# Kernel optimization log

Measured on AMD Instinct MI355X. Metric: run time of the kernel, lower is better.

Reference implementation:

```python
import jax, jax.numpy as jnp
import numpy as np

LN_EPS = 1e-5

def _layer_norm(x, g, b):
    mu = jnp.mean(x, axis=-1, keepdims=True)
    var = jnp.mean(jnp.square(x - mu), axis=-1, keepdims=True)
    return (x - mu) * jax.lax.rsqrt(var + LN_EPS) * g + b

def _conv(x, src, tgt, N, alphas, ws, W3, W_self, bias, deg_power):
    # alphas, ws: tuples of 3 per-edge [E] arrays (sp, ctx, lat)
    # W3: [3, in, out]; deg_power: [3]
    out = x @ W_self + bias  # self loop + bias, [N, out]
    for c in range(3):
        eff = alphas[c] * ws[c]                                   # [E]
        deg = jnp.ones((N,), x.dtype).at[tgt].add(eff)            # [N]
        dinv = jnp.power(jnp.clip(deg, 1e-6), deg_power[c])       # [N]
        norm = eff * dinv[tgt] * dinv[src]                        # [E]
        h = x @ W3[c]                                             # [N, out] (linear => transform before gather)
        msg = norm[:, None] * h[src]                              # [E, out]
        out = out + jax.ops.segment_sum(msg, tgt, num_segments=N)
    return out

def setup_inputs() -> dict:
    N, E, D, L = 50000, 1000000, 128, 2
    key = jax.random.key(0)
    ks = jax.random.split(key, 16)
    scale = 1.0 / np.sqrt(D)
    inp = {
        "x": jax.random.normal(ks[0], (N, D), jnp.float32),
        "edge_index": jax.random.randint(ks[1], (2, E), 0, N, jnp.int32),
        "alpha_sp": jax.random.uniform(ks[2], (E,), jnp.float32),
        "alpha_ctx": jax.random.uniform(ks[3], (E,), jnp.float32),
        "alpha_lat": jax.random.uniform(ks[4], (E,), jnp.float32),
        "w_sp": jax.random.uniform(ks[5], (E,), jnp.float32),
        "w_ctx": jax.random.uniform(ks[6], (E,), jnp.float32),
        "w_lat": jax.random.uniform(ks[7], (E,), jnp.float32),
        # stacked per-layer params: [L, 3, in, out] for the three channel weights
        "W3": jax.random.normal(ks[8], (L, 3, D, D), jnp.float32) * scale,
        "W_self": jax.random.normal(ks[9], (L, D, D), jnp.float32) * scale,
        "bias": jnp.zeros((L, D), jnp.float32),
        "deg_power": jnp.full((L, 3), -0.5, jnp.float32),
        "ln_g": jnp.ones((D,), jnp.float32),
        "ln_b": jnp.zeros((D,), jnp.float32),
        "num_nodes": N,
    }
    return inp

def reference(x, edge_index, alpha_sp, alpha_ctx, alpha_lat, w_sp, w_ctx, w_lat,
              W3, W_self, bias, deg_power, ln_g, ln_b, num_nodes):
    N = num_nodes
    src, tgt = edge_index[0], edge_index[1]
    alphas = (alpha_sp, alpha_ctx, alpha_lat)
    ws = (w_sp, w_ctx, w_lat)
    L = W3.shape[0]
    h = x
    for i in range(L):
        h = _conv(h, src, tgt, N, alphas, ws, W3[i], W_self[i], bias[i], deg_power[i])
        if i < L - 1:
            h = _layer_norm(h, ln_g, ln_b)
            h = jax.nn.relu(h)
            # dropout: eval mode (identity)
    return h
```

## Files before the change

kernel.cpp:

```cpp
#include <hip/hip_runtime.h>
#include <hip/hip_bf16.h>

typedef short bf16x8 __attribute__((ext_vector_type(8)));
typedef float f32x4 __attribute__((ext_vector_type(4)));

#define BSH 7
#define BK  (1 << BSH)

static inline int cdiv(int a, int b){ return (a + b - 1) / b; }

__device__ __forceinline__ unsigned pack_bf16_hi(float v){
    return ((unsigned)__bfloat16_as_ushort(__float2bfloat16(v))) << 16;
}
__device__ __forceinline__ float bf16hi_to_f32(unsigned bits_hi16){
    return __uint_as_float(bits_hi16);
}

__global__ __launch_bounds__(256) void k_bcnt0(const int* __restrict__ tgt,
                                               int* __restrict__ gcnt, int E, int NB){
    __shared__ int lh[1024];
    int tid = threadIdx.x;
    for (int b = tid; b < 1024; b += 256) lh[b] = 0;
    __syncthreads();
    int c0 = blockIdx.x * 4096;
    #pragma unroll
    for (int u = 0; u < 16; ++u){
        int e = c0 + u * 256 + tid;
        if (e < E) atomicAdd(&lh[tgt[e] >> BSH], 1);
    }
    __syncthreads();
    for (int b = tid; b < NB; b += 256){
        int c = lh[b];
        if (c) atomicAdd(&gcnt[b], c);
    }
}

__global__ __launch_bounds__(256) void k_bscan(const int* __restrict__ gcnt,
                                               int* __restrict__ bbase,
                                               int* __restrict__ gcur,
                                               int* __restrict__ rs,
                                               int N, int E){
    __shared__ int sc[256];
    int tid = threadIdx.x;
    int b0 = tid * 4;
    int v0 = gcnt[b0], v1 = gcnt[b0 + 1], v2 = gcnt[b0 + 2], v3 = gcnt[b0 + 3];
    int t3 = v0 + v1 + v2 + v3;
    sc[tid] = t3;
    __syncthreads();
    for (int off = 1; off < 256; off <<= 1){
        int x = (tid >= off) ? sc[tid - off] : 0;
        __syncthreads();
        sc[tid] += x;
        __syncthreads();
    }
    int ex = sc[tid] - t3;
    bbase[b0]     = ex;
    bbase[b0 + 1] = ex + v0;
    bbase[b0 + 2] = ex + v0 + v1;
    bbase[b0 + 3] = ex + v0 + v1 + v2;
    gcur[b0] = bbase[b0]; gcur[b0 + 1] = bbase[b0 + 1];
    gcur[b0 + 2] = bbase[b0 + 2]; gcur[b0 + 3] = bbase[b0 + 3];
    if (tid == 255) bbase[1024] = sc[255];
    if (tid == 0)   rs[N] = E;
}

__global__ __launch_bounds__(256) void k_bin(
        const int* __restrict__ src, const int* __restrict__ tgt,
        const float* __restrict__ asp, const float* __restrict__ actx,
        const float* __restrict__ alat, const float* __restrict__ wsp,
        const float* __restrict__ wctx, const float* __restrict__ wlat,
        int* __restrict__ gcur, uint4* __restrict__ binned, int E, int NB){
    __shared__ int lh[1024], lc[1024], gb[1024];
    int tid = threadIdx.x;
    int c0 = blockIdx.x * 4096;
    for (int b = tid; b < 1024; b += 256){ lh[b] = 0; lc[b] = 0; }
    __syncthreads();
    #pragma unroll
    for (int u = 0; u < 16; ++u){
        int e = c0 + u * 256 + tid;
        if (e < E) atomicAdd(&lh[tgt[e] >> BSH], 1);
    }
    __syncthreads();
    for (int b = tid; b < NB; b += 256){
        int c = lh[b];
        gb[b] = c ? atomicAdd(&gcur[b], c) : 0;
    }
    __syncthreads();
    #pragma unroll
    for (int u = 0; u < 16; ++u){
        int e = c0 + u * 256 + tid;
        if (e < E){
            int t = tgt[e];
            int b = t >> BSH;
            int p = gb[b] + atomicAdd(&lc[b], 1);
            uint4 o;
            o.x = (unsigned)src[e] | pack_bf16_hi(asp[e] * wsp[e]);
            o.y = (pack_bf16_hi(actx[e] * wctx[e]) >> 16) | pack_bf16_hi(alat[e] * wlat[e]);
            o.z = (unsigned)t;
            o.w = 0u;
            binned[p] = o;
        }
    }
}

__global__ __launch_bounds__(256) void k_bucket(
        const uint4* __restrict__ binned, const int* __restrict__ bbase,
        const float* __restrict__ dp,
        uint2* __restrict__ effo, int* __restrict__ rs,
        float* __restrict__ dinv_all,
        int N, int L){
    __shared__ int th[128], sc2[128], cur[128];
    __shared__ float sm[384];
    int tid = threadIdx.x;
    int b = blockIdx.x;
    int t0 = b << BSH;
    int ebeg = bbase[b], eend = bbase[b + 1];
    if (tid < 128) th[tid] = 0;
    for (int j = tid; j < 384; j += 256) sm[j] = 0.f;
    __syncthreads();
    for (int i = ebeg + tid; i < eend; i += 256)
        atomicAdd(&th[(int)binned[i].z - t0], 1);
    __syncthreads();
    int v = (tid < 128) ? th[tid] : 0;
    if (tid < 128) sc2[tid] = v;
    __syncthreads();
    for (int off = 1; off < 128; off <<= 1){
        int x = (tid >= off && tid < 128) ? sc2[tid - off] : 0;
        __syncthreads();
        if (tid < 128) sc2[tid] += x;
        __syncthreads();
    }
    if (tid < 128){
        int exv = sc2[tid] - v;
        cur[tid] = exv;
        int t = t0 + tid;
        if (t < N) rs[t] = ebeg + exv;
    }
    __syncthreads();
    for (int i = ebeg + tid; i < eend; i += 256){
        uint4 r = binned[i];
        int loc = (int)r.z - t0;
        int p = atomicAdd(&cur[loc], 1);
        uint2 o = {r.x, r.y};
        effo[ebeg + p] = o;
        atomicAdd(&sm[loc * 3 + 0], bf16hi_to_f32(r.x & 0xFFFF0000u));
        atomicAdd(&sm[loc * 3 + 1], bf16hi_to_f32(r.y << 16));
        atomicAdd(&sm[loc * 3 + 2], bf16hi_to_f32(r.y & 0xFFFF0000u));
    }
    __syncthreads();
    if (tid < 128){
        int t = t0 + tid;
        if (t < N){
            float d0 = fmaxf(1.f + sm[tid * 3 + 0], 1e-6f);
            float d1 = fmaxf(1.f + sm[tid * 3 + 1], 1e-6f);
            float d2 = fmaxf(1.f + sm[tid * 3 + 2], 1e-6f);
            for (int l = 0; l < L; ++l){
                size_t base = ((size_t)l * N + t) * 3;
                dinv_all[base + 0] = powf(d0, dp[l * 3 + 0]);
                dinv_all[base + 1] = powf(d1, dp[l * 3 + 1]);
                dinv_all[base + 2] = powf(d2, dp[l * 3 + 2]);
            }
        }
    }
}

__global__ void k_prep(const uint2* __restrict__ effo,
                       const float* __restrict__ dinv_all,
                       uint2* __restrict__ nv,
                       const float* __restrict__ x, __hip_bfloat16* __restrict__ xg,
                       const float* __restrict__ Wself, const float* __restrict__ W3,
                       __hip_bfloat16* __restrict__ BT,
                       int N, int E, int L){
    int gid = blockIdx.x * 256 + threadIdx.x;
    int LE = L * E;
    int nx4 = (N * 128) >> 2;
    int nw = L * 65536;
    if (gid < LE){
        int l = gid / E;
        int e = gid - l * E;
        const float* dinv = dinv_all + (size_t)l * N * 3;
        uint2 v = effo[e];
        unsigned s = v.x & 0xFFFFu;
        float e0 = bf16hi_to_f32(v.x & 0xFFFF0000u);
        float e1 = bf16hi_to_f32(v.y << 16);
        float e2 = bf16hi_to_f32(v.y & 0xFFFF0000u);
        uint2 o;
        o.x = s | pack_bf16_hi(e0 * dinv[3 * s + 0]);
        o.y = (pack_bf16_hi(e1 * dinv[3 * s + 1]) >> 16)
            | pack_bf16_hi(e2 * dinv[3 * s + 2]);
        nv[gid] = o;
    } else if (gid < LE + nx4){
        int i = gid - LE;
        float4 v = ((const float4*)x)[i];
        float2 lo = {v.x, v.y}, hi = {v.z, v.w};
        ((__hip_bfloat162*)xg)[2 * i]     = __float22bfloat162_rn(lo);
        ((__hip_bfloat162*)xg)[2 * i + 1] = __float22bfloat162_rn(hi);
    } else if (gid < LE + nx4 + nw){
        int q = gid - LE - nx4;
        int l = q >> 16, r = q & 65535;
        int j = r >> 9, k = r & 511;
        float v;
        if (k < 128) v = Wself[l * 16384 + k * 128 + j];
        else {
            int c = (k >> 7) - 1, kk = k & 127;
            v = W3[l * 49152 + (c * 128 + kk) * 128 + j];
        }
        BT[q] = __float2bfloat16(v);
    }
}

__global__ __launch_bounds__(256) void k_msg(
        const __hip_bfloat16* __restrict__ xg,
        __hip_bfloat16* __restrict__ Yg,
        const uint2* __restrict__ nv,
        const int* __restrict__ rs,
        const float* __restrict__ dinv,
        int N){
    int w = threadIdx.x >> 6, lane = threadIdx.x & 63;
    int t = blockIdx.x * 4 + w;
    if (t >= N) return;
    float ax0 = 0.f, ay0 = 0.f, ax1 = 0.f, ay1 = 0.f, ax2 = 0.f, ay2 = 0.f;
    int beg = rs[t], end = rs[t + 1];
    int i = beg;
    for (; i + 8 <= end; i += 8){
        uint2 m[8];
        #pragma unroll
        for (int u = 0; u < 8; ++u) m[u] = nv[i + u];
        float2 f[8];
        #pragma unroll
        for (int u = 0; u < 8; ++u){
            const __hip_bfloat162* p =
                (const __hip_bfloat162*)(xg + (size_t)(m[u].x & 0xFFFFu) * 128);
            f[u] = __bfloat1622float2(p[lane]);
        }
        #pragma unroll
        for (int u = 0; u < 8; ++u){
            float n0 = bf16hi_to_f32(m[u].x & 0xFFFF0000u);
            float n1 = bf16hi_to_f32(m[u].y << 16);
            float n2 = bf16hi_to_f32(m[u].y & 0xFFFF0000u);
            ax0 += n0 * f[u].x; ay0 += n0 * f[u].y;
            ax1 += n1 * f[u].x; ay1 += n1 * f[u].y;
            ax2 += n2 * f[u].x; ay2 += n2 * f[u].y;
        }
    }
    for (; i < end; ++i){
        uint2 m = nv[i];
        const __hip_bfloat162* p =
            (const __hip_bfloat162*)(xg + (size_t)(m.x & 0xFFFFu) * 128);
        float2 fv = __bfloat1622float2(p[lane]);
        float n0 = bf16hi_to_f32(m.x & 0xFFFF0000u);
        float n1 = bf16hi_to_f32(m.y << 16);
        float n2 = bf16hi_to_f32(m.y & 0xFFFF0000u);
        ax0 += n0 * fv.x; ay0 += n0 * fv.y;
        ax1 += n1 * fv.x; ay1 += n1 * fv.y;
        ax2 += n2 * fv.x; ay2 += n2 * fv.y;
    }
    float dt0 = dinv[3 * t], dt1 = dinv[3 * t + 1], dt2 = dinv[3 * t + 2];
    __hip_bfloat162* yo = (__hip_bfloat162*)(Yg + (size_t)t * 384) + lane;
    float2 r0 = {dt0 * ax0, dt0 * ay0};
    float2 r1 = {dt1 * ax1, dt1 * ay1};
    float2 r2 = {dt2 * ax2, dt2 * ay2};
    yo[0]   = __float22bfloat162_rn(r0);
    yo[64]  = __float22bfloat162_rn(r1);
    yo[128] = __float22bfloat162_rn(r2);
}

__global__ __launch_bounds__(256) void k_gemm(
        const __hip_bfloat16* __restrict__ Yg,
        const __hip_bfloat16* __restrict__ BT,
        const float* __restrict__ bias,
        float* __restrict__ outbuf,
        int M, int doLN,
        const float* __restrict__ g, const float* __restrict__ b,
        __hip_bfloat16* __restrict__ xg){
    __shared__ __hip_bfloat16 As[64 * 128];
    __shared__ __hip_bfloat16 Bs[128 * 128];
    const int tid = threadIdx.x;
    const int row0 = blockIdx.x * 64;
    const int w = tid >> 6, lane = tid & 63;
    const int wm = (w & 1) * 32, wn = (w >> 1) * 64;
    const int lm = lane & 15, lq = lane >> 4;

    f32x4 acc[2][4];
    #pragma unroll
    for (int mt = 0; mt < 2; ++mt)
        #pragma unroll
        for (int nt = 0; nt < 4; ++nt)
            acc[mt][nt] = {0.f, 0.f, 0.f, 0.f};

    for (int kt = 0; kt < 4; ++kt){
        #pragma unroll
        for (int it = 0; it < 4; ++it){
            int v = it * 256 + tid;
            int r = v >> 4, c = v & 15;
            int soff = r * 128 + ((c ^ (r & 15)) << 3);
            int4 av = {0, 0, 0, 0};
            if (row0 + r < M){
                if (kt == 0)
                    av = *(const int4*)(xg + (size_t)(row0 + r) * 128 + (c << 3));
                else
                    av = *(const int4*)(Yg + (size_t)(row0 + r) * 384
                                        + (kt - 1) * 128 + (c << 3));
            }
            *(int4*)(&As[soff]) = av;
        }
        #pragma unroll
        for (int it = 0; it < 8; ++it){
            int v = it * 256 + tid;
            int r = v >> 4, c = v & 15;
            int soff = r * 128 + ((c ^ (r & 15)) << 3);
            int4 bv = *(const int4*)(BT + (size_t)r * 512 + kt * 128 + (c << 3));
            *(int4*)(&Bs[soff]) = bv;
        }
        __syncthreads();

        #pragma unroll
        for (int kk = 0; kk < 4; ++kk){
            int kc = kk * 4 + lq;
            bf16x8 a[2], b2[4];
            #pragma unroll
            for (int mt = 0; mt < 2; ++mt){
                int r = wm + mt * 16 + lm;
                a[mt] = *(const bf16x8*)(&As[r * 128 + ((kc ^ (r & 15)) << 3)]);
            }
            #pragma unroll
            for (int nt = 0; nt < 4; ++nt){
                int r = wn + nt * 16 + lm;
                b2[nt] = *(const bf16x8*)(&Bs[r * 128 + ((kc ^ (r & 15)) << 3)]);
            }
            #pragma unroll
            for (int mt = 0; mt < 2; ++mt)
                #pragma unroll
                for (int nt = 0; nt < 4; ++nt)
                    acc[mt][nt] = __builtin_amdgcn_mfma_f32_16x16x32_bf16(
                        a[mt], b2[nt], acc[mt][nt], 0, 0, 0);
        }
        __syncthreads();
    }

    if (!doLN){
        #pragma unroll
        for (int mt = 0; mt < 2; ++mt){
            #pragma unroll
            for (int nt = 0; nt < 4; ++nt){
                int col = wn + nt * 16 + lm;
                #pragma unroll
                for (int r = 0; r < 4; ++r){
                    int row = row0 + wm + mt * 16 + lq * 4 + r;
                    if (row < M)
                        outbuf[(size_t)row * 128 + col] = acc[mt][nt][r] + bias[col];
                }
            }
        }
    } else {
        float* S1 = (float*)As;
        float* S2 = S1 + 2048;
        float* MS = (float*)Bs;
        const int half = wn >> 6;
        const int slot = half * 16 + lm;
        float bv[4];
        #pragma unroll
        for (int nt = 0; nt < 4; ++nt) bv[nt] = bias[wn + nt * 16 + lm];
        #pragma unroll
        for (int mt = 0; mt < 2; ++mt){
            #pragma unroll
            for (int r = 0; r < 4; ++r){
                int rl = wm + mt * 16 + lq * 4 + r;
                float ps = 0.f, pq = 0.f;
                #pragma unroll
                for (int nt = 0; nt < 4; ++nt){
                    float v = acc[mt][nt][r] + bv[nt];
                    ps += v; pq += v * v;
                }
                S1[rl * 32 + slot] = ps;
                S2[rl * 32 + slot] = pq;
            }
        }
        __syncthreads();
        if (tid < 64){
            float s = 0.f, sq = 0.f;
            #pragma unroll
            for (int j = 0; j < 32; ++j){
                s  += S1[tid * 32 + j];
                sq += S2[tid * 32 + j];
            }
            float mu = s * (1.0f / 128.0f);
            float var = sq * (1.0f / 128.0f) - mu * mu;
            MS[tid] = mu;
            MS[64 + tid] = rsqrtf(var + 1e-5f);
        }
        __syncthreads();
        float gv[4], bbv[4];
        #pragma unroll
        for (int nt = 0; nt < 4; ++nt){
            int col = wn + nt * 16 + lm;
            gv[nt] = g[col]; bbv[nt] = b[col];
        }
        #pragma unroll
        for (int mt = 0; mt < 2; ++mt){
            #pragma unroll
            for (int r = 0; r < 4; ++r){
                int rl = wm + mt * 16 + lq * 4 + r;
                int row = row0 + rl;
                if (row < M){
                    float mu = MS[rl], sc = MS[64 + rl];
                    #pragma unroll
                    for (int nt = 0; nt < 4; ++nt){
                        int col = wn + nt * 16 + lm;
                        float v = acc[mt][nt][r] + bv[nt];
                        float y = fmaxf((v - mu) * sc * gv[nt] + bbv[nt], 0.0f);
                        xg[(size_t)row * 128 + col] = __float2bfloat16(y);
                    }
                }
            }
        }
    }
}

extern "C" void kernel_launch(void* const* d_in, const int* in_sizes, int n_in,
                              void* d_out, int out_size, void* d_ws, size_t ws_size,
                              hipStream_t stream) {
    const float* x     = (const float*)d_in[0];
    const int*   ei    = (const int*)d_in[1];
    const float* asp   = (const float*)d_in[2];
    const float* actx  = (const float*)d_in[3];
    const float* alat  = (const float*)d_in[4];
    const float* wsp   = (const float*)d_in[5];
    const float* wctx  = (const float*)d_in[6];
    const float* wlat  = (const float*)d_in[7];
    const float* W3    = (const float*)d_in[8];
    const float* Wself = (const float*)d_in[9];
    const float* bias  = (const float*)d_in[10];
    const float* dpow  = (const float*)d_in[11];
    const float* lng   = (const float*)d_in[12];
    const float* lnb   = (const float*)d_in[13];

    const int N = in_sizes[0] / 128;
    const int E = in_sizes[1] / 2;
    const int L = in_sizes[8] / (3 * 128 * 128);
    const int NB = cdiv(N, BK);
    const int* src = ei;
    const int* tgt = ei + E;

    char* p = (char*)d_ws;
    auto alloc = [&](size_t bytes) -> void* {
        void* r = (void*)p;
        p += (bytes + 255) & ~(size_t)255;
        return r;
    };
    int*   rs       = (int*)  alloc((size_t)(N + 1) * 4);
    int*   gcnt     = (int*)  alloc(1024 * 4);
    int*   bbase    = (int*)  alloc(1025 * 4);
    int*   gcur     = (int*)  alloc(1024 * 4);
    uint2* effo     = (uint2*)alloc((size_t)E * 8);
    size_t nv_bytes = (size_t)L * E * 8, bn_bytes = (size_t)E * 16;
    uint2* nv       = (uint2*)alloc(nv_bytes > bn_bytes ? nv_bytes : bn_bytes);
    float* dinv_all = (float*)alloc((size_t)L * N * 3 * 4);
    __hip_bfloat16* xg = (__hip_bfloat16*)alloc((size_t)N * 128 * 2);
    __hip_bfloat16* Yg = (__hip_bfloat16*)alloc((size_t)N * 384 * 2);
    __hip_bfloat16* BT = (__hip_bfloat16*)alloc((size_t)L * 128 * 512 * 2);
    uint4* binned = (uint4*)nv;

    hipMemsetAsync(gcnt, 0, 1024 * 4, stream);
    k_bcnt0 <<<cdiv(E, 4096), 256, 0, stream>>>(tgt, gcnt, E, NB);
    k_bscan <<<1, 256, 0, stream>>>(gcnt, bbase, gcur, rs, N, E);
    k_bin   <<<cdiv(E, 4096), 256, 0, stream>>>(src, tgt, asp, actx, alat, wsp, wctx, wlat,
                                                gcur, binned, E, NB);
    k_bucket<<<NB, 256, 0, stream>>>(binned, bbase, dpow, effo, rs, dinv_all, N, L);
    {
        int total = L * E + ((N * 128) >> 2) + L * 65536;
        k_prep<<<cdiv(total, 256), 256, 0, stream>>>(effo, dinv_all, nv, x, xg,
                                                     Wself, W3, BT, N, E, L);
    }

    for (int l = 0; l < L; ++l){
        int doLN = (l < L - 1) ? 1 : 0;
        const float* dinv_l = dinv_all + (size_t)l * N * 3;
        k_msg <<<cdiv(N, 4), 256, 0, stream>>>(xg, Yg, nv + (size_t)l * E, rs, dinv_l, N);
        k_gemm<<<cdiv(N, 64), 256, 0, stream>>>(Yg, BT + (size_t)l * 65536,
                                                bias + l * 128, (float*)d_out, N,
                                                doLN, lng, lnb, xg);
    }
}
```

Measured before the change: 351.3 us.

## Replace two-level bucketed CSR build with direct per-node histogram, scan, scatter

Replaces the two-pass bucket binning (block-local histograms over 128-node buckets, then per-bucket sort with shared-memory degree sums) with a plain global atomic histogram over targets, a three-kernel prefix scan, a global-atomic scatter into CSR order, and a separate per-node degree kernel. This removes the intermediate 16-byte binned buffer and one full pass over it. In exchange it relies on global atomics spread across 50k counters, scatters with poor locality, and the degree kernel walks variable-length rows per thread. Edge order within a row is now nondeterministic, so the bf16 degree sums may vary slightly between runs.

```diff
diff --git a/kernel.cpp b/kernel.cpp
--- a/kernel.cpp
+++ b/kernel.cpp
@@ -4,9 +4,6 @@
 typedef short bf16x8 __attribute__((ext_vector_type(8)));
 typedef float f32x4 __attribute__((ext_vector_type(4)));
 
-#define BSH 7
-#define BK  (1 << BSH)
-
 static inline int cdiv(int a, int b){ return (a + b - 1) / b; }
 
 __device__ __forceinline__ unsigned pack_bf16_hi(float v){
@@ -16,34 +13,23 @@
     return __uint_as_float(bits_hi16);
 }
 
-__global__ __launch_bounds__(256) void k_bcnt0(const int* __restrict__ tgt,
-                                               int* __restrict__ gcnt, int E, int NB){
-    __shared__ int lh[1024];
-    int tid = threadIdx.x;
-    for (int b = tid; b < 1024; b += 256) lh[b] = 0;
-    __syncthreads();
-    int c0 = blockIdx.x * 4096;
-    #pragma unroll
-    for (int u = 0; u < 16; ++u){
-        int e = c0 + u * 256 + tid;
-        if (e < E) atomicAdd(&lh[tgt[e] >> BSH], 1);
-    }
-    __syncthreads();
-    for (int b = tid; b < NB; b += 256){
-        int c = lh[b];
-        if (c) atomicAdd(&gcnt[b], c);
-    }
-}
-
-__global__ __launch_bounds__(256) void k_bscan(const int* __restrict__ gcnt,
-                                               int* __restrict__ bbase,
-                                               int* __restrict__ gcur,
+__global__ __launch_bounds__(256) void k_hist(const int* __restrict__ tgt,
+                                              int* __restrict__ cnt, int E){
+    int stride = gridDim.x * 256;
+    for (int e = blockIdx.x * 256 + threadIdx.x; e < E; e += stride)
+        atomicAdd(&cnt[tgt[e]], 1);
+}
+
+__global__ __launch_bounds__(256) void k_scanA(const int* __restrict__ cnt,
                                                int* __restrict__ rs,
-                                               int N, int E){
+                                               int* __restrict__ part, int N){
     __shared__ int sc[256];
     int tid = threadIdx.x;
-    int b0 = tid * 4;
-    int v0 = gcnt[b0], v1 = gcnt[b0 + 1], v2 = gcnt[b0 + 2], v3 = gcnt[b0 + 3];
+    int base = blockIdx.x * 1024 + tid * 4;
+    int v0 = (base + 0 < N) ? cnt[base + 0] : 0;
+    int v1 = (base + 1 < N) ? cnt[base + 1] : 0;
+    int v2 = (base + 2 < N) ? cnt[base + 2] : 0;
+    int v3 = (base + 3 < N) ? cnt[base + 3] : 0;
     int t3 = v0 + v1 + v2 + v3;
     sc[tid] = t3;
     __syncthreads();
@@ -54,113 +40,74 @@
         __syncthreads();
     }
     int ex = sc[tid] - t3;
-    bbase[b0]     = ex;
-    bbase[b0 + 1] = ex + v0;
-    bbase[b0 + 2] = ex + v0 + v1;
-    bbase[b0 + 3] = ex + v0 + v1 + v2;
-    gcur[b0] = bbase[b0]; gcur[b0 + 1] = bbase[b0 + 1];
-    gcur[b0 + 2] = bbase[b0 + 2]; gcur[b0 + 3] = bbase[b0 + 3];
-    if (tid == 255) bbase[1024] = sc[255];
-    if (tid == 0)   rs[N] = E;
-}
-
-__global__ __launch_bounds__(256) void k_bin(
+    if (base + 0 < N) rs[base + 0] = ex;
+    if (base + 1 < N) rs[base + 1] = ex + v0;
+    if (base + 2 < N) rs[base + 2] = ex + v0 + v1;
+    if (base + 3 < N) rs[base + 3] = ex + v0 + v1 + v2;
+    if (tid == 255) part[blockIdx.x] = sc[255];
+}
+
+__global__ void k_scanB(int* __restrict__ part, int nb){
+    if (blockIdx.x == 0 && threadIdx.x == 0){
+        int acc = 0;
+        for (int i = 0; i < nb; ++i){ int t = part[i]; part[i] = acc; acc += t; }
+    }
+}
+
+__global__ __launch_bounds__(256) void k_scanC(int* __restrict__ rs,
+                                               int* __restrict__ cur,
+                                               const int* __restrict__ part,
+                                               int N, int E){
+    int i = blockIdx.x * 1024 + threadIdx.x * 4;
+    int b = part[blockIdx.x];
+    #pragma unroll
+    for (int u = 0; u < 4; ++u){
+        int j = i + u;
+        if (j < N){ int v = rs[j] + b; rs[j] = v; cur[j] = v; }
+    }
+    if (blockIdx.x == 0 && threadIdx.x == 0) rs[N] = E;
+}
+
+__global__ __launch_bounds__(256) void k_scatter(
         const int* __restrict__ src, const int* __restrict__ tgt,
         const float* __restrict__ asp, const float* __restrict__ actx,
         const float* __restrict__ alat, const float* __restrict__ wsp,
         const float* __restrict__ wctx, const float* __restrict__ wlat,
-        int* __restrict__ gcur, uint4* __restrict__ binned, int E, int NB){
-    __shared__ int lh[1024], lc[1024], gb[1024];
-    int tid = threadIdx.x;
-    int c0 = blockIdx.x * 4096;
-    for (int b = tid; b < 1024; b += 256){ lh[b] = 0; lc[b] = 0; }
-    __syncthreads();
-    #pragma unroll
-    for (int u = 0; u < 16; ++u){
-        int e = c0 + u * 256 + tid;
-        if (e < E) atomicAdd(&lh[tgt[e] >> BSH], 1);
-    }
-    __syncthreads();
-    for (int b = tid; b < NB; b += 256){
-        int c = lh[b];
-        gb[b] = c ? atomicAdd(&gcur[b], c) : 0;
-    }
-    __syncthreads();
-    #pragma unroll
-    for (int u = 0; u < 16; ++u){
-        int e = c0 + u * 256 + tid;
-        if (e < E){
-            int t = tgt[e];
-            int b = t >> BSH;
-            int p = gb[b] + atomicAdd(&lc[b], 1);
-            uint4 o;
-            o.x = (unsigned)src[e] | pack_bf16_hi(asp[e] * wsp[e]);
-            o.y = (pack_bf16_hi(actx[e] * wctx[e]) >> 16) | pack_bf16_hi(alat[e] * wlat[e]);
-            o.z = (unsigned)t;
-            o.w = 0u;
-            binned[p] = o;
-        }
-    }
-}
-
-__global__ __launch_bounds__(256) void k_bucket(
-        const uint4* __restrict__ binned, const int* __restrict__ bbase,
+        int* __restrict__ cur, uint2* __restrict__ effo, int E){
+    int stride = gridDim.x * 256;
+    for (int e = blockIdx.x * 256 + threadIdx.x; e < E; e += stride){
+        int t = tgt[e];
+        int p = atomicAdd(&cur[t], 1);
+        uint2 o;
+        o.x = (unsigned)src[e] | pack_bf16_hi(asp[e] * wsp[e]);
+        o.y = (pack_bf16_hi(actx[e] * wctx[e]) >> 16) | pack_bf16_hi(alat[e] * wlat[e]);
+        effo[p] = o;
+    }
+}
+
+__global__ __launch_bounds__(256) void k_deg(
+        const uint2* __restrict__ effo, const int* __restrict__ rs,
         const float* __restrict__ dp,
-        uint2* __restrict__ effo, int* __restrict__ rs,
         float* __restrict__ dinv_all,
         int N, int L){
-    __shared__ int th[128], sc2[128], cur[128];
-    __shared__ float sm[384];
-    int tid = threadIdx.x;
-    int b = blockIdx.x;
-    int t0 = b << BSH;
-    int ebeg = bbase[b], eend = bbase[b + 1];
-    if (tid < 128) th[tid] = 0;
-    for (int j = tid; j < 384; j += 256) sm[j] = 0.f;
-    __syncthreads();
-    for (int i = ebeg + tid; i < eend; i += 256)
-        atomicAdd(&th[(int)binned[i].z - t0], 1);
-    __syncthreads();
-    int v = (tid < 128) ? th[tid] : 0;
-    if (tid < 128) sc2[tid] = v;
-    __syncthreads();
-    for (int off = 1; off < 128; off <<= 1){
-        int x = (tid >= off && tid < 128) ? sc2[tid - off] : 0;
-        __syncthreads();
-        if (tid < 128) sc2[tid] += x;
-        __syncthreads();
-    }
-    if (tid < 128){
-        int exv = sc2[tid] - v;
-        cur[tid] = exv;
-        int t = t0 + tid;
-        if (t < N) rs[t] = ebeg + exv;
-    }
-    __syncthreads();
-    for (int i = ebeg + tid; i < eend; i += 256){
-        uint4 r = binned[i];
-        int loc = (int)r.z - t0;
-        int p = atomicAdd(&cur[loc], 1);
-        uint2 o = {r.x, r.y};
-        effo[ebeg + p] = o;
-        atomicAdd(&sm[loc * 3 + 0], bf16hi_to_f32(r.x & 0xFFFF0000u));
-        atomicAdd(&sm[loc * 3 + 1], bf16hi_to_f32(r.y << 16));
-        atomicAdd(&sm[loc * 3 + 2], bf16hi_to_f32(r.y & 0xFFFF0000u));
-    }
-    __syncthreads();
-    if (tid < 128){
-        int t = t0 + tid;
-        if (t < N){
-            float d0 = fmaxf(1.f + sm[tid * 3 + 0], 1e-6f);
-            float d1 = fmaxf(1.f + sm[tid * 3 + 1], 1e-6f);
-            float d2 = fmaxf(1.f + sm[tid * 3 + 2], 1e-6f);
-            for (int l = 0; l < L; ++l){
-                size_t base = ((size_t)l * N + t) * 3;
-                dinv_all[base + 0] = powf(d0, dp[l * 3 + 0]);
-                dinv_all[base + 1] = powf(d1, dp[l * 3 + 1]);
-                dinv_all[base + 2] = powf(d2, dp[l * 3 + 2]);
-            }
-        }
+    int n = blockIdx.x * 256 + threadIdx.x;
+    if (n >= N) return;
+    int beg = rs[n], end = rs[n + 1];
+    float s0 = 0.f, s1 = 0.f, s2 = 0.f;
+    for (int i = beg; i < end; ++i){
+        uint2 v = effo[i];
+        s0 += bf16hi_to_f32(v.x & 0xFFFF0000u);
+        s1 += bf16hi_to_f32(v.y << 16);
+        s2 += bf16hi_to_f32(v.y & 0xFFFF0000u);
+    }
+    float d0 = fmaxf(1.f + s0, 1e-6f);
+    float d1 = fmaxf(1.f + s1, 1e-6f);
+    float d2 = fmaxf(1.f + s2, 1e-6f);
+    for (int l = 0; l < L; ++l){
+        size_t base = ((size_t)l * N + n) * 3;
+        dinv_all[base + 0] = powf(d0, dp[l * 3 + 0]);
+        dinv_all[base + 1] = powf(d1, dp[l * 3 + 1]);
+        dinv_all[base + 2] = powf(d2, dp[l * 3 + 2]);
     }
 }
 
@@ -438,7 +385,6 @@
     const int N = in_sizes[0] / 128;
     const int E = in_sizes[1] / 2;
     const int L = in_sizes[8] / (3 * 128 * 128);
-    const int NB = cdiv(N, BK);
     const int* src = ei;
     const int* tgt = ei + E;
 
@@ -449,24 +395,26 @@
         return r;
     };
     int*   rs       = (int*)  alloc((size_t)(N + 1) * 4);
-    int*   gcnt     = (int*)  alloc(1024 * 4);
-    int*   bbase    = (int*)  alloc(1025 * 4);
-    int*   gcur     = (int*)  alloc(1024 * 4);
+    int*   cnt      = (int*)  alloc((size_t)N * 4);
+    int*   cur      = (int*)  alloc((size_t)N * 4);
+    int*   part     = (int*)  alloc(256 * 4);
     uint2* effo     = (uint2*)alloc((size_t)E * 8);
-    size_t nv_bytes = (size_t)L * E * 8, bn_bytes = (size_t)E * 16;
-    uint2* nv       = (uint2*)alloc(nv_bytes > bn_bytes ? nv_bytes : bn_bytes);
+    uint2* nv       = (uint2*)alloc((size_t)L * E * 8);
     float* dinv_all = (float*)alloc((size_t)L * N * 3 * 4);
     __hip_bfloat16* xg = (__hip_bfloat16*)alloc((size_t)N * 128 * 2);
     __hip_bfloat16* Yg = (__hip_bfloat16*)alloc((size_t)N * 384 * 2);
     __hip_bfloat16* BT = (__hip_bfloat16*)alloc((size_t)L * 128 * 512 * 2);
-    uint4* binned = (uint4*)nv;
-
-    hipMemsetAsync(gcnt, 0, 1024 * 4, stream);
-    k_bcnt0 <<<cdiv(E, 4096), 256, 0, stream>>>(tgt, gcnt, E, NB);
-    k_bscan <<<1, 256, 0, stream>>>(gcnt, bbase, gcur, rs, N, E);
-    k_bin   <<<cdiv(E, 4096), 256, 0, stream>>>(src, tgt, asp, actx, alat, wsp, wctx, wlat,
-                                                gcur, binned, E, NB);
-    k_bucket<<<NB, 256, 0, stream>>>(binned, bbase, dpow, effo, rs, dinv_all, N, L);
+
+    const int nb = cdiv(N, 1024);
+
+    hipMemsetAsync(cnt, 0, (size_t)N * 4, stream);
+    k_hist   <<<2048, 256, 0, stream>>>(tgt, cnt, E);
+    k_scanA  <<<nb, 256, 0, stream>>>(cnt, rs, part, N);
+    k_scanB  <<<1, 64, 0, stream>>>(part, nb);
+    k_scanC  <<<nb, 256, 0, stream>>>(rs, cur, part, N, E);
+    k_scatter<<<2048, 256, 0, stream>>>(src, tgt, asp, actx, alat, wsp, wctx, wlat,
+                                        cur, effo, E);
+    k_deg    <<<cdiv(N, 256), 256, 0, stream>>>(effo, rs, dpow, dinv_all, N, L);
     {
         int total = L * E + ((N * 128) >> 2) + L * 65536;
         k_prep<<<cdiv(total, 256), 256, 0, stream>>>(effo, dinv_all, nv, x, xg,
```

Result: slower. 398.2 us (+13.3%).
